# Kernel optimization log

Hardware: AMD Instinct MI355X
Metric: run time of the kernel (lower is better)

## Reference

```python
import jax, jax.numpy as jnp
import numpy as np

N_NODES = 100000
N_EDGES = 1600000
IN_F = 128
HID_F = 128
N_CLS = 40


def _linear_params(key, out_f, in_f):
    k1, k2 = jax.random.split(key)
    s = 1.0 / np.sqrt(in_f)
    w = jax.random.uniform(k1, (out_f, in_f), jnp.float32, -s, s)
    b = jax.random.uniform(k2, (out_f,), jnp.float32, -s, s)
    return w, b


def setup_inputs() -> dict:
    key = jax.random.key(0)
    ks = jax.random.split(key, 9)
    in_feat = jax.random.normal(ks[0], (N_NODES, IN_F), jnp.float32)
    src = jax.random.randint(ks[1], (N_EDGES,), 0, N_NODES, jnp.int32)
    dst = jax.random.randint(ks[2], (N_EDGES,), 0, N_NODES, jnp.int32)
    pool_w1, pool_b1 = _linear_params(ks[3], IN_F, IN_F)
    self_w1, self_b1 = _linear_params(ks[4], HID_F, IN_F)
    neigh_w1, neigh_b1 = _linear_params(ks[5], HID_F, IN_F)
    pool_w2, pool_b2 = _linear_params(ks[6], HID_F, HID_F)
    self_w2, self_b2 = _linear_params(ks[7], N_CLS, HID_F)
    neigh_w2, neigh_b2 = _linear_params(ks[8], N_CLS, HID_F)
    return dict(in_feat=in_feat, src=src, dst=dst,
                pool_w1=pool_w1, pool_b1=pool_b1, self_w1=self_w1, self_b1=self_b1,
                neigh_w1=neigh_w1, neigh_b1=neigh_b1,
                pool_w2=pool_w2, pool_b2=pool_b2, self_w2=self_w2, self_b2=self_b2,
                neigh_w2=neigh_w2, neigh_b2=neigh_b2)


def sage_conv_pool(h, src, dst, pool_w, pool_b, self_w, self_b, neigh_w, neigh_b):
    # fc_pool + relu on nodes first (N < E), then gather per edge
    m = jax.nn.relu(h @ pool_w.T + pool_b)            # [N, d]
    msgs = m[src]                                     # [E, d] gather
    agg = jax.ops.segment_max(msgs, dst, num_segments=N_NODES)  # [N, d]
    agg = jnp.where(jnp.isfinite(agg), agg, 0.0)      # zero for isolated nodes
    return h @ self_w.T + self_b + agg @ neigh_w.T + neigh_b


def reference(in_feat, src, dst,
              pool_w1, pool_b1, self_w1, self_b1, neigh_w1, neigh_b1,
              pool_w2, pool_b2, self_w2, self_b2, neigh_w2, neigh_b2):
    h = sage_conv_pool(in_feat, src, dst, pool_w1, pool_b1, self_w1, self_b1, neigh_w1, neigh_b1)
    h = jax.nn.relu(h)  # dropout is identity in eval mode
    h = sage_conv_pool(h, src, dst, pool_w2, pool_b2, self_w2, self_b2, neigh_w2, neigh_b2)
    return h
```

## Files before the change

kernel.cpp:

```cpp
#include <hip/hip_runtime.h>


#define N_FEAT 128
#define NWG_A 256
#define BSHIFT 10
#define NBMAX 128

typedef __attribute__((ext_vector_type(8))) short bf16x8;
typedef __attribute__((ext_vector_type(8))) unsigned short u16x8;
typedef __attribute__((ext_vector_type(4))) float f32x4;

static __device__ __forceinline__ unsigned short f2bf(float f) {
    unsigned u = __float_as_uint(f);
    unsigned r = (u + 0x7fffu + ((u >> 16) & 1u)) >> 16;
    return (unsigned short)r;
}

static __device__ __forceinline__ bf16x8 loadA_f32(const float* __restrict__ A, size_t idx) {
    float4 a = *(const float4*)&A[idx];
    float4 b = *(const float4*)&A[idx + 4];
    bf16x8 r;
    r[0] = (short)f2bf(a.x); r[1] = (short)f2bf(a.y);
    r[2] = (short)f2bf(a.z); r[3] = (short)f2bf(a.w);
    r[4] = (short)f2bf(b.x); r[5] = (short)f2bf(b.y);
    r[6] = (short)f2bf(b.z); r[7] = (short)f2bf(b.w);
    return r;
}

__global__ __launch_bounds__(256) void prep_bin_kernel(
    const float* __restrict__ pw1, const float* __restrict__ sw1,
    const float* __restrict__ nw1, const float* __restrict__ pw2,
    const float* __restrict__ sw2, const float* __restrict__ nw2,
    const float* __restrict__ sb1, const float* __restrict__ nb1,
    const float* __restrict__ sb2, const float* __restrict__ nb2,
    unsigned short* __restrict__ wb_p1, unsigned short* __restrict__ wb_s1,
    unsigned short* __restrict__ wb_n1, unsigned short* __restrict__ wb_p2,
    unsigned short* __restrict__ wb_s2, unsigned short* __restrict__ wb_n2,
    float* __restrict__ b_sn1, float* __restrict__ b_sn2,
    const int* __restrict__ dst, int* __restrict__ wgcnt, int E, int NB)
{
    __shared__ int cnt[NBMAX];
    if (blockIdx.x < NWG_A) {
        const int wg = blockIdx.x, tid = threadIdx.x;
        if (tid < NB) cnt[tid] = 0;
        __syncthreads();
        const int slab = (E + NWG_A - 1) / NWG_A;
        const int e0 = wg * slab;
        const int e1 = min(e0 + slab, E);
        for (int e = e0 + tid; e < e1; e += 256)
            atomicAdd(&cnt[dst[e] >> BSHIFT], 1);
        __syncthreads();
        if (tid < NB) wgcnt[tid * NWG_A + wg] = cnt[tid];
    } else {
        int t = (blockIdx.x - NWG_A) * 256 + threadIdx.x;
        if (t < 16384) {
            wb_p1[t] = f2bf(pw1[t]);
            wb_s1[t] = f2bf(sw1[t]);
            wb_n1[t] = f2bf(nw1[t]);
            wb_p2[t] = f2bf(pw2[t]);
        }
        if (t < 6144) {
            int row = t >> 7;
            wb_s2[t] = (row < 40) ? f2bf(sw2[t]) : 0;
            wb_n2[t] = (row < 40) ? f2bf(nw2[t]) : 0;
        }
        if (t < 128) b_sn1[t] = sb1[t] + nb1[t];
        if (t < 64)  b_sn2[t] = (t < 40) ? (sb2[t] + nb2[t]) : 0.f;
    }
}

__global__ __launch_bounds__(1024) void bin_scan_kernel(const int* __restrict__ wgcnt,
                                                        int* __restrict__ binoff, int NB)
{
    __shared__ int sh[1024];
    const int t = threadIdx.x;
    const int total = NB * NWG_A;
    const int chunk = (total + 1023) / 1024;
    const int b0 = t * chunk;
    const int b1 = min(b0 + chunk, total);
    int s = 0;
    for (int k = b0; k < b1; k++) s += wgcnt[k];
    sh[t] = s;
    __syncthreads();
    for (int off = 1; off < 1024; off <<= 1) {
        int x = (t >= off) ? sh[t - off] : 0;
        __syncthreads();
        sh[t] += x;
        __syncthreads();
    }
    int run = sh[t] - s;
    for (int k = b0; k < b1; k++) {
        int v = wgcnt[k];
        binoff[k] = run;
        run += v;
    }
    if (t == 1023) binoff[total] = sh[1023];
}

__global__ __launch_bounds__(256, 4) void scatter_pool_kernel(
    const int* __restrict__ src, const int* __restrict__ dst,
    const int* __restrict__ binoff, unsigned* __restrict__ binned, int E, int NB,
    const float* __restrict__ A0f, const unsigned short* __restrict__ B0,
    const float* __restrict__ bias, unsigned short* __restrict__ Cout, int M)
{
    __shared__ int cur[NBMAX];
    __shared__ unsigned short Bs[128 * 136];
    __shared__ float BsF[128];

    if (blockIdx.x < NWG_A) {
        const int wg = blockIdx.x, tid = threadIdx.x;
        if (tid < NB) cur[tid] = binoff[tid * NWG_A + wg];
        __syncthreads();
        const int slab = (E + NWG_A - 1) / NWG_A;
        const int e0 = wg * slab;
        const int e1 = min(e0 + slab, E);
        for (int e = e0 + tid; e < e1; e += 256) {
            int d = dst[e];
            int b = d >> BSHIFT;
            unsigned rec = ((unsigned)(d & ((1 << BSHIFT) - 1)) << 17) | (unsigned)src[e];
            int p = atomicAdd(&cur[b], 1);
            binned[p] = rec;
        }
        return;
    }

    const int tid = threadIdx.x;
    const int w = tid >> 6, lane = tid & 63;
    const int q = lane >> 4, r16 = lane & 15;
    const int m0 = (blockIdx.x - NWG_A) * 128;

    if (tid < 128) BsF[tid] = bias[tid];

    int rowA[2];
#pragma unroll
    for (int rt = 0; rt < 2; rt++) {
        int r = m0 + w * 32 + rt * 16 + r16;
        rowA[rt] = r < M ? r : (M - 1);
    }

    f32x4 acc[2][8];
#pragma unroll
    for (int i = 0; i < 2; i++)
#pragma unroll
        for (int j = 0; j < 8; j++) acc[i][j] = (f32x4){0.f, 0.f, 0.f, 0.f};

    for (int j = tid; j < 2048; j += 256) {
        int row = j >> 4, cc = j & 15;
        *(uint4*)&Bs[row * 136 + cc * 8] = *(const uint4*)&B0[(size_t)row * 128 + cc * 8];
    }
    __syncthreads();

#pragma unroll
    for (int k0 = 0; k0 < 128; k0 += 32) {
        bf16x8 af[2];
#pragma unroll
        for (int rt = 0; rt < 2; rt++)
            af[rt] = loadA_f32(A0f, (size_t)rowA[rt] * 128 + k0 + q * 8);
#pragma unroll
        for (int ct = 0; ct < 8; ct++) {
            bf16x8 bfr = *(const bf16x8*)&Bs[(ct * 16 + r16) * 136 + k0 + q * 8];
#pragma unroll
            for (int rt = 0; rt < 2; rt++)
                acc[rt][ct] = __builtin_amdgcn_mfma_f32_16x16x32_bf16(
                    af[rt], bfr, acc[rt][ct], 0, 0, 0);
        }
    }

#pragma unroll
    for (int rt = 0; rt < 2; rt++) {
#pragma unroll
        for (int ct = 0; ct < 8; ct++) {
            int col = ct * 16 + r16;
#pragma unroll
            for (int r = 0; r < 4; r++) {
                int grow = m0 + w * 32 + rt * 16 + q * 4 + r;
                if (grow < M) {
                    float v = fmaxf(acc[rt][ct][r] + BsF[col], 0.f);
                    Cout[(size_t)grow * 128 + col] = f2bf(v);
                }
            }
        }
    }
}

__global__ __launch_bounds__(1024) void csr_build_kernel(const unsigned* __restrict__ binned,
                                                         const int* __restrict__ binoff,
                                                         int* __restrict__ csr,
                                                         int* __restrict__ offsets,
                                                         int* __restrict__ counts, int M)
{
    __shared__ int cnt[1 << BSHIFT];
    __shared__ int pref[1 << BSHIFT];
    const int b = blockIdx.x, t = threadIdx.x;
    const int rs = binoff[b * NWG_A];
    const int re = binoff[(b + 1) * NWG_A];

    cnt[t] = 0;
    __syncthreads();
    for (int i = rs + t; i < re; i += 1024)
        atomicAdd(&cnt[binned[i] >> 17], 1);
    __syncthreads();

    int v = cnt[t];
    pref[t] = v;
    __syncthreads();
    for (int off = 1; off < 1024; off <<= 1) {
        int x = (t >= off) ? pref[t - off] : 0;
        __syncthreads();
        pref[t] += x;
        __syncthreads();
    }
    int excl = pref[t] - v;

    int node = (b << BSHIFT) + t;
    if (node < M) {
        counts[node] = v;
        offsets[node] = rs + excl;
    }
    cnt[t] = excl;
    __syncthreads();

    for (int i = rs + t; i < re; i += 1024) {
        unsigned r = binned[i];
        int p = atomicAdd(&cnt[r >> 17], 1);
        csr[rs + p] = (int)(r & 0x1FFFFu);
    }
}

__global__ __launch_bounds__(256) void gather_max_kernel(
    const u16x8* __restrict__ m16, const int* __restrict__ csr,
    const int* __restrict__ offsets, const int* __restrict__ counts,
    u16x8* __restrict__ agg16, int Nn)
{
    int wid = (blockIdx.x * 256 + threadIdx.x) >> 6;
    int lane = threadIdx.x & 63;
    if (wid >= Nn) return;
    const int g = lane >> 4, c = lane & 15;
    int start = offsets[wid];
    int deg = counts[wid];
    u16x8 acc = (u16x8){0, 0, 0, 0, 0, 0, 0, 0};
    for (int j0 = 0; j0 < deg; j0 += 64) {
        int nb = deg - j0;
        if (nb > 64) nb = 64;
        int sl = csr[start + j0 + (lane < nb ? lane : nb - 1)];
        for (int j = 0; j < nb; j += 4) {
            int jj = j + g;
            if (jj >= nb) jj = nb - 1;
            int s = __shfl(sl, jj);
            u16x8 v = m16[(size_t)s * 16 + c];
            acc = __builtin_elementwise_max(acc, v);
        }
    }
#pragma unroll
    for (int d = 16; d <= 32; d <<= 1) {
        int4 a = *(int4*)&acc;
        int4 t;
        t.x = __shfl_xor(a.x, d);
        t.y = __shfl_xor(a.y, d);
        t.z = __shfl_xor(a.z, d);
        t.w = __shfl_xor(a.w, d);
        acc = __builtin_elementwise_max(acc, *(u16x8*)&t);
    }
    if (g == 0) __builtin_nontemporal_store(acc, &agg16[(size_t)wid * 16 + c]);
}

template<int NT, bool RELU, int NPAIRS, bool F32OUT>
__global__ __launch_bounds__(256, 4) void mfma_gemm_kernel(
    const unsigned short* __restrict__ A0, const unsigned short* __restrict__ B0,
    const unsigned short* __restrict__ A1, const unsigned short* __restrict__ B1,
    const float* __restrict__ bias, void* __restrict__ Cout, int M, int Nout)
{
    constexpr int NR = NT * 16;
    __shared__ unsigned short Bs[NR * 136];
    __shared__ float BsF[NR];

    const int tid = threadIdx.x;
    const int w = tid >> 6, lane = tid & 63;
    const int q = lane >> 4, r16 = lane & 15;
    const int m0 = blockIdx.x * 128;

    if (tid < NR) BsF[tid] = (tid < Nout) ? bias[tid] : 0.f;

    int rowA[2];
#pragma unroll
    for (int rt = 0; rt < 2; rt++) {
        int r = m0 + w * 32 + rt * 16 + r16;
        rowA[rt] = r < M ? r : (M - 1);
    }

    f32x4 acc[2][NT];
#pragma unroll
    for (int i = 0; i < 2; i++)
#pragma unroll
        for (int j = 0; j < NT; j++) acc[i][j] = (f32x4){0.f, 0.f, 0.f, 0.f};

    for (int p = 0; p < NPAIRS; p++) {
        const unsigned short* __restrict__ B = p ? B1 : B0;
        const unsigned short* __restrict__ A = p ? A1 : A0;
        if (p) __syncthreads();
        for (int j = tid; j < NR * 16; j += 256) {
            int row = j >> 4, cc = j & 15;
            uint4 v = *(const uint4*)&B[(size_t)row * 128 + cc * 8];
            *(uint4*)&Bs[row * 136 + cc * 8] = v;
        }
        __syncthreads();

#pragma unroll
        for (int k0 = 0; k0 < 128; k0 += 32) {
            bf16x8 af[2];
#pragma unroll
            for (int rt = 0; rt < 2; rt++)
                af[rt] = *(const bf16x8*)&A[(size_t)rowA[rt] * 128 + k0 + q * 8];
#pragma unroll
            for (int ct = 0; ct < NT; ct++) {
                bf16x8 bfr = *(const bf16x8*)&Bs[(ct * 16 + r16) * 136 + k0 + q * 8];
#pragma unroll
                for (int rt = 0; rt < 2; rt++)
                    acc[rt][ct] = __builtin_amdgcn_mfma_f32_16x16x32_bf16(
                        af[rt], bfr, acc[rt][ct], 0, 0, 0);
            }
        }
    }

#pragma unroll
    for (int rt = 0; rt < 2; rt++) {
#pragma unroll
        for (int ct = 0; ct < NT; ct++) {
            int col = ct * 16 + r16;
#pragma unroll
            for (int r = 0; r < 4; r++) {
                int grow = m0 + w * 32 + rt * 16 + q * 4 + r;
                float v = acc[rt][ct][r] + BsF[col];
                if (RELU) v = fmaxf(v, 0.f);
                if (grow < M && col < Nout) {
                    if (F32OUT)
                        ((float*)Cout)[(size_t)grow * Nout + col] = v;
                    else
                        ((unsigned short*)Cout)[(size_t)grow * Nout + col] = f2bf(v);
                }
            }
        }
    }
}

__global__ __launch_bounds__(256, 3) void sn_pool_kernel(
    const float* __restrict__ A0f, const unsigned short* __restrict__ B0,
    const unsigned short* __restrict__ A1, const unsigned short* __restrict__ B1,
    const float* __restrict__ bias_sn, const unsigned short* __restrict__ Bp,
    const float* __restrict__ bias_p, unsigned short* __restrict__ h1out,
    unsigned short* __restrict__ m2out, int M)
{
    __shared__ unsigned short Bs[128 * 72];
    __shared__ unsigned short H[128 * 136];
    __shared__ float BsF[128];

    const int tid = threadIdx.x;
    const int w = tid >> 6, lane = tid & 63;
    const int q = lane >> 4, r16 = lane & 15;
    const int m0 = blockIdx.x * 128;

    if (tid < 128) BsF[tid] = bias_sn[tid];

    int rowA[2];
#pragma unroll
    for (int rt = 0; rt < 2; rt++) {
        int r = m0 + w * 32 + rt * 16 + r16;
        rowA[rt] = r < M ? r : (M - 1);
    }

    f32x4 acc[2][8];
#pragma unroll
    for (int i = 0; i < 2; i++)
#pragma unroll
        for (int j = 0; j < 8; j++) acc[i][j] = (f32x4){0.f, 0.f, 0.f, 0.f};

    for (int p = 0; p < 2; p++) {
        const unsigned short* __restrict__ B = p ? B1 : B0;
        for (int kh = 0; kh < 2; kh++) {
            __syncthreads();
            for (int j = tid; j < 1024; j += 256) {
                int row = j >> 3, cc = j & 7;
                *(uint4*)&Bs[row * 72 + cc * 8] =
                    *(const uint4*)&B[(size_t)row * 128 + kh * 64 + cc * 8];
            }
            __syncthreads();
#pragma unroll
            for (int k0i = 0; k0i < 2; k0i++) {
                const int k0 = kh * 64 + k0i * 32;
                const int koff = k0i * 32;
                bf16x8 af[2];
#pragma unroll
                for (int rt = 0; rt < 2; rt++) {
                    if (p == 0)
                        af[rt] = loadA_f32(A0f, (size_t)rowA[rt] * 128 + k0 + q * 8);
                    else
                        af[rt] = *(const bf16x8*)&A1[(size_t)rowA[rt] * 128 + k0 + q * 8];
                }
#pragma unroll
                for (int ct = 0; ct < 8; ct++) {
                    bf16x8 bfr = *(const bf16x8*)&Bs[(ct * 16 + r16) * 72 + koff + q * 8];
#pragma unroll
                    for (int rt = 0; rt < 2; rt++)
                        acc[rt][ct] = __builtin_amdgcn_mfma_f32_16x16x32_bf16(
                            af[rt], bfr, acc[rt][ct], 0, 0, 0);
                }
            }
        }
    }

#pragma unroll
    for (int rt = 0; rt < 2; rt++) {
#pragma unroll
        for (int ct = 0; ct < 8; ct++) {
            int col = ct * 16 + r16;
#pragma unroll
            for (int r = 0; r < 4; r++) {
                int lr = w * 32 + rt * 16 + q * 4 + r;
                int grow = m0 + lr;
                float v = fmaxf(acc[rt][ct][r] + BsF[col], 0.f);
                unsigned short hb = f2bf(v);
                H[lr * 136 + col] = hb;
                if (grow < M) h1out[(size_t)grow * 128 + col] = hb;
            }
        }
    }
    __syncthreads();
    if (tid < 128) BsF[tid] = bias_p[tid];

#pragma unroll
    for (int i = 0; i < 2; i++)
#pragma unroll
        for (int j = 0; j < 8; j++) acc[i][j] = (f32x4){0.f, 0.f, 0.f, 0.f};

    for (int kh = 0; kh < 2; kh++) {
        __syncthreads();
        for (int j = tid; j < 1024; j += 256) {
            int row = j >> 3, cc = j & 7;
            *(uint4*)&Bs[row * 72 + cc * 8] =
                *(const uint4*)&Bp[(size_t)row * 128 + kh * 64 + cc * 8];
        }
        __syncthreads();
#pragma unroll
        for (int k0i = 0; k0i < 2; k0i++) {
            const int k0 = kh * 64 + k0i * 32;
            const int koff = k0i * 32;
            bf16x8 af[2];
#pragma unroll
            for (int rt = 0; rt < 2; rt++)
                af[rt] = *(const bf16x8*)&H[(w * 32 + rt * 16 + r16) * 136 + k0 + q * 8];
#pragma unroll
            for (int ct = 0; ct < 8; ct++) {
                bf16x8 bfr = *(const bf16x8*)&Bs[(ct * 16 + r16) * 72 + koff + q * 8];
#pragma unroll
                for (int rt = 0; rt < 2; rt++)
                    acc[rt][ct] = __builtin_amdgcn_mfma_f32_16x16x32_bf16(
                        af[rt], bfr, acc[rt][ct], 0, 0, 0);
            }
        }
    }

#pragma unroll
    for (int rt = 0; rt < 2; rt++) {
#pragma unroll
        for (int ct = 0; ct < 8; ct++) {
            int col = ct * 16 + r16;
#pragma unroll
            for (int r = 0; r < 4; r++) {
                int grow = m0 + w * 32 + rt * 16 + q * 4 + r;
                if (grow < M) {
                    float v = fmaxf(acc[rt][ct][r] + BsF[col], 0.f);
                    m2out[(size_t)grow * 128 + col] = f2bf(v);
                }
            }
        }
    }
}

extern "C" void kernel_launch(void* const* d_in, const int* in_sizes, int n_in,
                              void* d_out, int out_size, void* d_ws, size_t ws_size,
                              hipStream_t stream)
{
    const float* in_feat = (const float*)d_in[0];
    const int*   src     = (const int*)d_in[1];
    const int*   dst     = (const int*)d_in[2];
    const float* pw1 = (const float*)d_in[3];  const float* pb1 = (const float*)d_in[4];
    const float* sw1 = (const float*)d_in[5];  const float* sb1 = (const float*)d_in[6];
    const float* nw1 = (const float*)d_in[7];  const float* nb1 = (const float*)d_in[8];
    const float* pw2 = (const float*)d_in[9];  const float* pb2 = (const float*)d_in[10];
    const float* sw2 = (const float*)d_in[11]; const float* sb2 = (const float*)d_in[12];
    const float* nw2 = (const float*)d_in[13]; const float* nb2 = (const float*)d_in[14];
    float* out = (float*)d_out;

    const int M = in_sizes[0] / N_FEAT;
    const int E = in_sizes[1];
    const int NB = (M + (1 << BSHIFT) - 1) >> BSHIFT;

    char* base = (char*)d_ws;
    size_t off = 0;
    auto alloc = [&](size_t bytes) { char* p = base + off; off = (off + bytes + 255) & ~(size_t)255; return p; };
    unsigned short* wb_p1 = (unsigned short*)alloc(16384 * 2);
    unsigned short* wb_s1 = (unsigned short*)alloc(16384 * 2);
    unsigned short* wb_n1 = (unsigned short*)alloc(16384 * 2);
    unsigned short* wb_p2 = (unsigned short*)alloc(16384 * 2);
    unsigned short* wb_s2 = (unsigned short*)alloc(6144 * 2);
    unsigned short* wb_n2 = (unsigned short*)alloc(6144 * 2);
    float* b_sn1 = (float*)alloc(128 * 4);
    float* b_sn2 = (float*)alloc(64 * 4);
    unsigned short* mb   = (unsigned short*)alloc((size_t)M * 128 * 2);
    unsigned short* agg  = (unsigned short*)alloc((size_t)M * 128 * 2);
    unsigned short* h1   = (unsigned short*)alloc((size_t)M * 128 * 2);
    int* counts  = (int*)alloc((size_t)M * 4);
    int* offsets = (int*)alloc((size_t)M * 4);
    int* wgcnt   = (int*)alloc((size_t)NB * NWG_A * 4);
    int* binoff  = (int*)alloc(((size_t)NB * NWG_A + 1) * 4);
    unsigned* binned = (unsigned*)alloc((size_t)E * 4);
    int* csr     = (int*)alloc((size_t)E * 4);

    const int gemm_grid = (M + 127) / 128;
    const int gather_grid = (M * 64 + 255) / 256;

    prep_bin_kernel<<<NWG_A + 64, 256, 0, stream>>>(
        pw1, sw1, nw1, pw2, sw2, nw2, sb1, nb1, sb2, nb2,
        wb_p1, wb_s1, wb_n1, wb_p2, wb_s2, wb_n2, b_sn1, b_sn2,
        dst, wgcnt, E, NB);
    bin_scan_kernel<<<1, 1024, 0, stream>>>(wgcnt, binoff, NB);
    scatter_pool_kernel<<<NWG_A + gemm_grid, 256, 0, stream>>>(
        src, dst, binoff, binned, E, NB,
        in_feat, wb_p1, pb1, mb, M);
    csr_build_kernel<<<NB, 1024, 0, stream>>>(binned, binoff, csr, offsets, counts, M);

    gather_max_kernel<<<gather_grid, 256, 0, stream>>>(
        (const u16x8*)mb, csr, offsets, counts, (u16x8*)agg, M);
    sn_pool_kernel<<<gemm_grid, 256, 0, stream>>>(
        in_feat, wb_s1, agg, wb_n1, b_sn1, wb_p2, pb2, h1, mb, M);

    gather_max_kernel<<<gather_grid, 256, 0, stream>>>(
        (const u16x8*)mb, csr, offsets, counts, (u16x8*)agg, M);
    mfma_gemm_kernel<3, false, 2, true><<<gemm_grid, 256, 0, stream>>>(
        h1, wb_s2, agg, wb_n2, b_sn2, out, M, 40);
}
```

Measured before the change: 373.4 us.

## Fuse layer-2 self projection into layer-1 kernel, drop h1 buffer

The layer-2 self projection (h1 @ self_w2 plus bias) is now computed inside sn_pool_kernel straight from the shared-memory H tile, and the partial result is written to the output. This removes the h1 round trip to global memory: a bf16 write of the full hidden matrix and its later read. The final kernel now only reads the existing output, adds agg @ neigh_w2, and writes it back. In exchange the output is stored twice and read once, and sn_pool_kernel does more work per block, which raises its register pressure.

```diff
diff --git a/kernel.cpp b/kernel.cpp
--- a/kernel.cpp
+++ b/kernel.cpp
@@ -264,23 +264,19 @@
     if (g == 0) __builtin_nontemporal_store(acc, &agg16[(size_t)wid * 16 + c]);
 }
 
-template<int NT, bool RELU, int NPAIRS, bool F32OUT>
-__global__ __launch_bounds__(256, 4) void mfma_gemm_kernel(
-    const unsigned short* __restrict__ A0, const unsigned short* __restrict__ B0,
-    const unsigned short* __restrict__ A1, const unsigned short* __restrict__ B1,
-    const float* __restrict__ bias, void* __restrict__ Cout, int M, int Nout)
-{
+__global__ __launch_bounds__(256, 4) void out_acc_kernel(
+    const unsigned short* __restrict__ agg, const unsigned short* __restrict__ Bn,
+    float* __restrict__ out, int M)
+{
+    constexpr int NT = 3;
     constexpr int NR = NT * 16;
     __shared__ unsigned short Bs[NR * 136];
-    __shared__ float BsF[NR];
 
     const int tid = threadIdx.x;
     const int w = tid >> 6, lane = tid & 63;
     const int q = lane >> 4, r16 = lane & 15;
     const int m0 = blockIdx.x * 128;
 
-    if (tid < NR) BsF[tid] = (tid < Nout) ? bias[tid] : 0.f;
-
     int rowA[2];
 #pragma unroll
     for (int rt = 0; rt < 2; rt++) {
@@ -288,40 +284,12 @@
         rowA[rt] = r < M ? r : (M - 1);
     }
 
+    for (int j = tid; j < NR * 16; j += 256) {
+        int row = j >> 4, cc = j & 15;
+        *(uint4*)&Bs[row * 136 + cc * 8] = *(const uint4*)&Bn[(size_t)row * 128 + cc * 8];
+    }
+
     f32x4 acc[2][NT];
-#pragma unroll
-    for (int i = 0; i < 2; i++)
-#pragma unroll
-        for (int j = 0; j < NT; j++) acc[i][j] = (f32x4){0.f, 0.f, 0.f, 0.f};
-
-    for (int p = 0; p < NPAIRS; p++) {
-        const unsigned short* __restrict__ B = p ? B1 : B0;
-        const unsigned short* __restrict__ A = p ? A1 : A0;
-        if (p) __syncthreads();
-        for (int j = tid; j < NR * 16; j += 256) {
-            int row = j >> 4, cc = j & 15;
-            uint4 v = *(const uint4*)&B[(size_t)row * 128 + cc * 8];
-            *(uint4*)&Bs[row * 136 + cc * 8] = v;
-        }
-        __syncthreads();
-
-#pragma unroll
-        for (int k0 = 0; k0 < 128; k0 += 32) {
-            bf16x8 af[2];
-#pragma unroll
-            for (int rt = 0; rt < 2; rt++)
-                af[rt] = *(const bf16x8*)&A[(size_t)rowA[rt] * 128 + k0 + q * 8];
-#pragma unroll
-            for (int ct = 0; ct < NT; ct++) {
-                bf16x8 bfr = *(const bf16x8*)&Bs[(ct * 16 + r16) * 136 + k0 + q * 8];
-#pragma unroll
-                for (int rt = 0; rt < 2; rt++)
-                    acc[rt][ct] = __builtin_amdgcn_mfma_f32_16x16x32_bf16(
-                        af[rt], bfr, acc[rt][ct], 0, 0, 0);
-            }
-        }
-    }
-
 #pragma unroll
     for (int rt = 0; rt < 2; rt++) {
 #pragma unroll
@@ -330,14 +298,38 @@
 #pragma unroll
             for (int r = 0; r < 4; r++) {
                 int grow = m0 + w * 32 + rt * 16 + q * 4 + r;
-                float v = acc[rt][ct][r] + BsF[col];
-                if (RELU) v = fmaxf(v, 0.f);
-                if (grow < M && col < Nout) {
-                    if (F32OUT)
-                        ((float*)Cout)[(size_t)grow * Nout + col] = v;
-                    else
-                        ((unsigned short*)Cout)[(size_t)grow * Nout + col] = f2bf(v);
-                }
+                acc[rt][ct][r] = (grow < M && col < 40) ? out[(size_t)grow * 40 + col] : 0.f;
+            }
+        }
+    }
+    __syncthreads();
+
+#pragma unroll
+    for (int k0 = 0; k0 < 128; k0 += 32) {
+        bf16x8 af[2];
+#pragma unroll
+        for (int rt = 0; rt < 2; rt++)
+            af[rt] = *(const bf16x8*)&agg[(size_t)rowA[rt] * 128 + k0 + q * 8];
+#pragma unroll
+        for (int ct = 0; ct < NT; ct++) {
+            bf16x8 bfr = *(const bf16x8*)&Bs[(ct * 16 + r16) * 136 + k0 + q * 8];
+#pragma unroll
+            for (int rt = 0; rt < 2; rt++)
+                acc[rt][ct] = __builtin_amdgcn_mfma_f32_16x16x32_bf16(
+                    af[rt], bfr, acc[rt][ct], 0, 0, 0);
+        }
+    }
+
+#pragma unroll
+    for (int rt = 0; rt < 2; rt++) {
+#pragma unroll
+        for (int ct = 0; ct < NT; ct++) {
+            int col = ct * 16 + r16;
+#pragma unroll
+            for (int r = 0; r < 4; r++) {
+                int grow = m0 + w * 32 + rt * 16 + q * 4 + r;
+                if (grow < M && col < 40)
+                    out[(size_t)grow * 40 + col] = acc[rt][ct][r];
             }
         }
     }
@@ -347,8 +339,9 @@
     const float* __restrict__ A0f, const unsigned short* __restrict__ B0,
     const unsigned short* __restrict__ A1, const unsigned short* __restrict__ B1,
     const float* __restrict__ bias_sn, const unsigned short* __restrict__ Bp,
-    const float* __restrict__ bias_p, unsigned short* __restrict__ h1out,
-    unsigned short* __restrict__ m2out, int M)
+    const float* __restrict__ bias_p, const unsigned short* __restrict__ Bs2,
+    const float* __restrict__ bias_sn2, unsigned short* __restrict__ m2out,
+    float* __restrict__ outp, int M)
 {
     __shared__ unsigned short Bs[128 * 72];
     __shared__ unsigned short H[128 * 136];
@@ -416,11 +409,8 @@
 #pragma unroll
             for (int r = 0; r < 4; r++) {
                 int lr = w * 32 + rt * 16 + q * 4 + r;
-                int grow = m0 + lr;
                 float v = fmaxf(acc[rt][ct][r] + BsF[col], 0.f);
-                unsigned short hb = f2bf(v);
-                H[lr * 136 + col] = hb;
-                if (grow < M) h1out[(size_t)grow * 128 + col] = hb;
+                H[lr * 136 + col] = f2bf(v);
             }
         }
     }
@@ -471,6 +461,54 @@
                     float v = fmaxf(acc[rt][ct][r] + BsF[col], 0.f);
                     m2out[(size_t)grow * 128 + col] = f2bf(v);
                 }
+            }
+        }
+    }
+
+    f32x4 acc2[2][3];
+#pragma unroll
+    for (int i = 0; i < 2; i++)
+#pragma unroll
+        for (int j = 0; j < 3; j++) acc2[i][j] = (f32x4){0.f, 0.f, 0.f, 0.f};
+
+    for (int kh = 0; kh < 2; kh++) {
+        __syncthreads();
+        for (int j = tid; j < 384; j += 256) {
+            int row = j >> 3, cc = j & 7;
+            *(uint4*)&Bs[row * 72 + cc * 8] =
+                *(const uint4*)&Bs2[(size_t)row * 128 + kh * 64 + cc * 8];
+        }
+        if (kh == 0 && tid < 64) BsF[tid] = bias_sn2[tid];
+        __syncthreads();
+#pragma unroll
+        for (int k0i = 0; k0i < 2; k0i++) {
+            const int k0 = kh * 64 + k0i * 32;
+            const int koff = k0i * 32;
+            bf16x8 af[2];
+#pragma unroll
+            for (int rt = 0; rt < 2; rt++)
+                af[rt] = *(const bf16x8*)&H[(w * 32 + rt * 16 + r16) * 136 + k0 + q * 8];
+#pragma unroll
+            for (int ct = 0; ct < 3; ct++) {
+                bf16x8 bfr = *(const bf16x8*)&Bs[(ct * 16 + r16) * 72 + koff + q * 8];
+#pragma unroll
+                for (int rt = 0; rt < 2; rt++)
+                    acc2[rt][ct] = __builtin_amdgcn_mfma_f32_16x16x32_bf16(
+                        af[rt], bfr, acc2[rt][ct], 0, 0, 0);
+            }
+        }
+    }
+
+#pragma unroll
+    for (int rt = 0; rt < 2; rt++) {
+#pragma unroll
+        for (int ct = 0; ct < 3; ct++) {
+            int col = ct * 16 + r16;
+#pragma unroll
+            for (int r = 0; r < 4; r++) {
+                int grow = m0 + w * 32 + rt * 16 + q * 4 + r;
+                if (grow < M && col < 40)
+                    outp[(size_t)grow * 40 + col] = acc2[rt][ct][r] + BsF[col];
             }
         }
     }
@@ -508,7 +546,6 @@
     float* b_sn2 = (float*)alloc(64 * 4);
     unsigned short* mb   = (unsigned short*)alloc((size_t)M * 128 * 2);
     unsigned short* agg  = (unsigned short*)alloc((size_t)M * 128 * 2);
-    unsigned short* h1   = (unsigned short*)alloc((size_t)M * 128 * 2);
     int* counts  = (int*)alloc((size_t)M * 4);
     int* offsets = (int*)alloc((size_t)M * 4);
     int* wgcnt   = (int*)alloc((size_t)NB * NWG_A * 4);
@@ -532,10 +569,10 @@
     gather_max_kernel<<<gather_grid, 256, 0, stream>>>(
         (const u16x8*)mb, csr, offsets, counts, (u16x8*)agg, M);
     sn_pool_kernel<<<gemm_grid, 256, 0, stream>>>(
-        in_feat, wb_s1, agg, wb_n1, b_sn1, wb_p2, pb2, h1, mb, M);
+        in_feat, wb_s1, agg, wb_n1, b_sn1, wb_p2, pb2,
+        wb_s2, b_sn2, mb, out, M);
 
     gather_max_kernel<<<gather_grid, 256, 0, stream>>>(
         (const u16x8*)mb, csr, offsets, counts, (u16x8*)agg, M);
-    mfma_gemm_kernel<3, false, 2, true><<<gemm_grid, 256, 0, stream>>>(
-        h1, wb_s2, agg, wb_n2, b_sn2, out, M, 40);
-}
+    out_acc_kernel<<<gemm_grid, 256, 0, stream>>>(agg, wb_n2, out, M);
+}
```

Result: no change. 375.1 us (+0.4%).
